# Performance work log

Measured on AMD Instinct MI355X. Metric: run time of the kernel, lower is better.

The kernel has to match this reference:

```python
import jax, jax.numpy as jnp
import numpy as np

N, F, H, E, G, C = 100000, 128, 128, 640000, 512, 6
EPS = 1e-5


def setup_inputs() -> dict:
    key = jax.random.key(0)
    ks = jax.random.split(key, 20)
    def w(k, shape, fan_in):
        return jax.random.normal(k, shape, jnp.float32) * (1.0 / np.sqrt(fan_in))
    return {
        "x": jax.random.normal(ks[0], (N, F), jnp.float32),
        "edge_index": jax.random.randint(ks[1], (2, E), 0, N),
        "batch": jnp.sort(jax.random.randint(ks[2], (N,), 0, G)),
        "num_graphs": G,
        # SAGEConv1: lin_l (aggregated, with bias) + lin_r (root, no bias)
        "W1l": w(ks[3], (F, H), F), "b1l": jnp.zeros((H,), jnp.float32), "W1r": w(ks[4], (F, H), F),
        # SAGEConv2
        "W2l": w(ks[5], (H, H), H), "b2l": jnp.zeros((H,), jnp.float32), "W2r": w(ks[6], (H, H), H),
        # cluster heads
        "Wc1": w(ks[7], (H, H), H), "bc1": jnp.zeros((H,), jnp.float32),
        "Wc2": w(ks[8], (H, 2), H), "bc2": jnp.zeros((2,), jnp.float32),
        # classifier
        "Wl1": w(ks[9], (H, H), H), "bl1": jnp.zeros((H,), jnp.float32),
        "Wl2": w(ks[10], (H, C), H), "bl2": jnp.zeros((C,), jnp.float32),
    }


def _sage(x, src, dst, Wl, bl, Wr):
    # PyG SAGEConv: mean-aggregate messages x[src] at dst, then lin_l(agg) + lin_r(x)
    n = x.shape[0]
    s = jax.ops.segment_sum(x[src], dst, num_segments=n)
    cnt = jax.ops.segment_sum(jnp.ones((src.shape[0],), x.dtype), dst, num_segments=n)
    agg = s / jnp.maximum(cnt, 1.0)[:, None]
    return agg @ Wl + bl + x @ Wr


def reference(x, edge_index, batch, num_graphs,
              W1l, b1l, W1r, W2l, b2l, W2r,
              Wc1, bc1, Wc2, bc2, Wl1, bl1, Wl2, bl2):
    src, dst = edge_index[0], edge_index[1]
    h = jax.nn.relu(_sage(x, src, dst, W1l, b1l, W1r))
    h = jax.nn.relu(_sage(h, src, dst, W2l, b2l, W2r))
    # 2-way soft cluster assignment per node
    a = jax.nn.softmax(jnp.tanh(h @ Wc1 + bc1) @ Wc2 + bc2, axis=1)  # [N,2]
    g = num_graphs
    # group_features[g] = a_g^T h_g  -> per-node outer product, segment-summed by graph
    gf = jax.ops.segment_sum(a[:, :, None] * h[:, None, :], batch, num_segments=g)  # [G,2,H]
    pos = gf[:, 0, :]  # positive-cluster embedding per graph
    # new_adj[g] = a_g^T A_g a_g ; only within-graph edges appear in the per-graph adj block
    same = (batch[src] == batch[dst]).astype(h.dtype)
    contrib = same[:, None, None] * (a[src][:, :, None] * a[dst][:, None, :])  # [E,2,2]
    new_adj = jax.ops.segment_sum(contrib, batch[src], num_segments=g)  # [G,2,2]
    # F.normalize(p=1, dim=1, eps=1e-5): row-wise L1 with clamped denominator
    l1 = jnp.sum(jnp.abs(new_adj), axis=2, keepdims=True)
    norm_adj = new_adj / jnp.maximum(l1, EPS)
    diag = jnp.diagonal(norm_adj, axis1=1, axis2=2)  # [G,2]
    penalty = jnp.mean(jnp.mean((diag - 1.0) ** 2, axis=1))  # mse vs ones(2), averaged over graphs
    # NOTE: original (faithfully reproduced) takes the mean over ALL nodes, same for every graph
    graph_emb = jnp.broadcast_to(jnp.mean(h, axis=0, keepdims=True), (g, h.shape[1]))
    z = jax.nn.relu(pos @ Wl1 + bl1)  # dropout off (eval mode)
    logits = z @ Wl2 + bl2
    return (jax.nn.log_softmax(logits, axis=-1), pos, graph_emb, penalty)
```

## Files before the change

kernel.cpp:

```cpp
#include <hip/hip_runtime.h>

#define NN 100000
#define NE 640000
#define HD 128
#define NG 512
#define NC 6
#define EPSV 1e-5f
#define OCT 12500

typedef __bf16 bf16_t;
typedef bf16_t bf16x8 __attribute__((ext_vector_type(8)));
typedef float f32x4 __attribute__((ext_vector_type(4)));

__device__ __forceinline__ float b2f(unsigned int u16) {
    return __builtin_bit_cast(float, u16 << 16);
}
__device__ __forceinline__ unsigned short f2b(float f) {
    unsigned int u = __builtin_bit_cast(unsigned int, f);
    unsigned int r = (u + 0x7fffu + ((u >> 16) & 1u)) >> 16;
    return (unsigned short)r;
}

__device__ __forceinline__ int frag_src(int i) {
    int g2 = i >> 6, ln = i & 63;
    int row = (g2 >> 2) * 16 + (ln & 15);
    return row * 16 + (g2 & 3) * 4 + (ln >> 4);
}

__global__ __launch_bounds__(256) void k_zero(uint4* __restrict__ p, int n16) {
    int i = blockIdx.x * 256 + threadIdx.x;
    if (i < n16) p[i] = (uint4){0u, 0u, 0u, 0u};
}

__global__ __launch_bounds__(256) void k_prep(
    const float* __restrict__ x, unsigned short* __restrict__ xb,
    const float* __restrict__ Wa, const float* __restrict__ Wb,
    const float* __restrict__ Wc, const float* __restrict__ Wd,
    const float* __restrict__ We, unsigned short* __restrict__ Wt,
    const int* __restrict__ dst, int* __restrict__ cnt)
{
    int bid = blockIdx.x;
    if (bid < 960) {
        int oct = bid & 7;
        int widx = bid >> 3;
        int lo = oct * OCT, hi = lo + OCT;
        for (int e = widx * 256 + threadIdx.x; e < NE; e += 120 * 256) {
            int d = dst[e];
            if (d >= lo && d < hi) atomicAdd(&cnt[d], 1);
        }
    } else if (bid < 7210) {
        int i = (bid - 960) * 256 + threadIdx.x;
        float4 v0 = reinterpret_cast<const float4*>(x)[i * 2];
        float4 v1 = reinterpret_cast<const float4*>(x)[i * 2 + 1];
        unsigned short u[8] = {f2b(v0.x), f2b(v0.y), f2b(v0.z), f2b(v0.w),
                               f2b(v1.x), f2b(v1.y), f2b(v1.z), f2b(v1.w)};
        reinterpret_cast<uint4*>(xb)[i] = *reinterpret_cast<uint4*>(u);
    } else {
        int i = (bid - 7210) * 256 + threadIdx.x;
        int w = i >> 14, r = i & 16383;
        int k = r >> 7, n = r & 127;
        const float* W = (w == 0) ? Wa : (w == 1) ? Wb : (w == 2) ? Wc : (w == 3) ? Wd : We;
        Wt[w * 16384 + n * HD + k] = f2b(W[k * HD + n]);
    }
}

__global__ void k_scan1(const int* __restrict__ cnt, int* __restrict__ excl,
                        int* __restrict__ bsum, int n) {
    __shared__ int sh[256];
    int i = blockIdx.x * 256 + threadIdx.x;
    int v = (i < n) ? cnt[i] : 0;
    sh[threadIdx.x] = v;
    __syncthreads();
    for (int off = 1; off < 256; off <<= 1) {
        int t = (threadIdx.x >= off) ? sh[threadIdx.x - off] : 0;
        __syncthreads();
        sh[threadIdx.x] += t;
        __syncthreads();
    }
    if (i < n) excl[i] = sh[threadIdx.x] - v;
    if (threadIdx.x == 255) bsum[blockIdx.x] = sh[255];
}

__global__ void k_scan2(int* bsum, int nb) {
    __shared__ int sh[512];
    int t = threadIdx.x;
    sh[t] = (t < nb) ? bsum[t] : 0;
    __syncthreads();
    for (int off = 1; off < 512; off <<= 1) {
        int v = (t >= off) ? sh[t - off] : 0;
        __syncthreads();
        sh[t] += v;
        __syncthreads();
    }
    if (t < nb) bsum[t] = sh[t];
}

__global__ void k_scan3(const int* __restrict__ excl, const int* __restrict__ bsum,
                        int* __restrict__ row_off, int n) {
    int i = blockIdx.x * 256 + threadIdx.x;
    if (i < n) row_off[i] = excl[i] + (blockIdx.x ? bsum[blockIdx.x - 1] : 0);
    if (i == 0) row_off[n] = NE;
}

__global__ __launch_bounds__(256) void k_fill(const int* __restrict__ src,
                                              const int* __restrict__ dst,
                                              const int* __restrict__ row_off,
                                              int* __restrict__ cnt,
                                              int* __restrict__ csr) {
    int q = blockIdx.x;
    int oct = q & 7;
    int widx = q >> 3;
    int lo = oct * OCT, hi = lo + OCT;
    for (int e = widx * 256 + threadIdx.x; e < NE; e += 120 * 256) {
        int d = dst[e];
        if (d >= lo && d < hi) {
            int p = atomicSub(&cnt[d], 1);
            csr[row_off[d] + p - 1] = src[e];
        }
    }
}

__global__ __launch_bounds__(512) void k_sage(
    const unsigned short* __restrict__ X,
    const int* __restrict__ row_off, const int* __restrict__ csr,
    const unsigned short* __restrict__ Wlt, const unsigned short* __restrict__ Wrt,
    const float* __restrict__ bias, unsigned short* __restrict__ out, int M)
{
    __shared__ uint4 wlds[4096];
    const int wid = threadIdx.x >> 6;
    const int lane = threadIdx.x & 63;
    const int lrow = lane & 15;
    const int lkg = lane >> 4;
    const int r0 = blockIdx.x * 128 + wid * 16;

    const uint4* gl = reinterpret_cast<const uint4*>(Wlt);
    const uint4* gr = reinterpret_cast<const uint4*>(Wrt);
    for (int i = threadIdx.x; i < 2048; i += 512) {
        int si = frag_src(i);
        wlds[i] = gl[si];
        wlds[2048 + i] = gr[si];
    }

    int row = r0 + lrow;
    row = row < M ? row : M - 1;
    int beg = row_off[row], end = row_off[row + 1];

    float accg[4][8];
#pragma unroll
    for (int ks = 0; ks < 4; ++ks)
#pragma unroll
        for (int j = 0; j < 8; ++j) accg[ks][j] = 0.f;

    const unsigned short* Xk = X + lkg * 8;
    for (int j = beg; j < end; j += 2) {
        int s0 = csr[j];
        const unsigned short* p0 = Xk + (size_t)s0 * HD;
        uint4 w0 = *reinterpret_cast<const uint4*>(p0);
        uint4 w1 = *reinterpret_cast<const uint4*>(p0 + 32);
        uint4 w2 = *reinterpret_cast<const uint4*>(p0 + 64);
        uint4 w3 = *reinterpret_cast<const uint4*>(p0 + 96);
        bool ok1 = (j + 1) < end;
        int s1 = csr[ok1 ? j + 1 : j];
        const unsigned short* p1 = Xk + (size_t)s1 * HD;
        uint4 y0, y1, y2, y3;
        if (ok1) {
            y0 = *reinterpret_cast<const uint4*>(p1);
            y1 = *reinterpret_cast<const uint4*>(p1 + 32);
            y2 = *reinterpret_cast<const uint4*>(p1 + 64);
            y3 = *reinterpret_cast<const uint4*>(p1 + 96);
        }
        accg[0][0] += b2f(w0.x & 0xffffu); accg[0][1] += b2f(w0.x >> 16);
        accg[0][2] += b2f(w0.y & 0xffffu); accg[0][3] += b2f(w0.y >> 16);
        accg[0][4] += b2f(w0.z & 0xffffu); accg[0][5] += b2f(w0.z >> 16);
        accg[0][6] += b2f(w0.w & 0xffffu); accg[0][7] += b2f(w0.w >> 16);
        accg[1][0] += b2f(w1.x & 0xffffu); accg[1][1] += b2f(w1.x >> 16);
        accg[1][2] += b2f(w1.y & 0xffffu); accg[1][3] += b2f(w1.y >> 16);
        accg[1][4] += b2f(w1.z & 0xffffu); accg[1][5] += b2f(w1.z >> 16);
        accg[1][6] += b2f(w1.w & 0xffffu); accg[1][7] += b2f(w1.w >> 16);
        accg[2][0] += b2f(w2.x & 0xffffu); accg[2][1] += b2f(w2.x >> 16);
        accg[2][2] += b2f(w2.y & 0xffffu); accg[2][3] += b2f(w2.y >> 16);
        accg[2][4] += b2f(w2.z & 0xffffu); accg[2][5] += b2f(w2.z >> 16);
        accg[2][6] += b2f(w2.w & 0xffffu); accg[2][7] += b2f(w2.w >> 16);
        accg[3][0] += b2f(w3.x & 0xffffu); accg[3][1] += b2f(w3.x >> 16);
        accg[3][2] += b2f(w3.y & 0xffffu); accg[3][3] += b2f(w3.y >> 16);
        accg[3][4] += b2f(w3.z & 0xffffu); accg[3][5] += b2f(w3.z >> 16);
        accg[3][6] += b2f(w3.w & 0xffffu); accg[3][7] += b2f(w3.w >> 16);
        if (ok1) {
            accg[0][0] += b2f(y0.x & 0xffffu); accg[0][1] += b2f(y0.x >> 16);
            accg[0][2] += b2f(y0.y & 0xffffu); accg[0][3] += b2f(y0.y >> 16);
            accg[0][4] += b2f(y0.z & 0xffffu); accg[0][5] += b2f(y0.z >> 16);
            accg[0][6] += b2f(y0.w & 0xffffu); accg[0][7] += b2f(y0.w >> 16);
            accg[1][0] += b2f(y1.x & 0xffffu); accg[1][1] += b2f(y1.x >> 16);
            accg[1][2] += b2f(y1.y & 0xffffu); accg[1][3] += b2f(y1.y >> 16);
            accg[1][4] += b2f(y1.z & 0xffffu); accg[1][5] += b2f(y1.z >> 16);
            accg[1][6] += b2f(y1.w & 0xffffu); accg[1][7] += b2f(y1.w >> 16);
            accg[2][0] += b2f(y2.x & 0xffffu); accg[2][1] += b2f(y2.x >> 16);
            accg[2][2] += b2f(y2.y & 0xffffu); accg[2][3] += b2f(y2.y >> 16);
            accg[2][4] += b2f(y2.z & 0xffffu); accg[2][5] += b2f(y2.z >> 16);
            accg[2][6] += b2f(y2.w & 0xffffu); accg[2][7] += b2f(y2.w >> 16);
            accg[3][0] += b2f(y3.x & 0xffffu); accg[3][1] += b2f(y3.x >> 16);
            accg[3][2] += b2f(y3.y & 0xffffu); accg[3][3] += b2f(y3.y >> 16);
            accg[3][4] += b2f(y3.z & 0xffffu); accg[3][5] += b2f(y3.z >> 16);
            accg[3][6] += b2f(y3.w & 0xffffu); accg[3][7] += b2f(y3.w >> 16);
        }
    }

    float inv = 1.f / fmaxf((float)(end - beg), 1.f);
    bf16x8 a1[4], a2f[4];
#pragma unroll
    for (int ks = 0; ks < 4; ++ks) {
        unsigned short u[8];
#pragma unroll
        for (int j = 0; j < 8; ++j) u[j] = f2b(accg[ks][j] * inv);
        a1[ks] = *reinterpret_cast<bf16x8*>(u);
    }
    const unsigned short* p2 = X + (size_t)row * HD + lkg * 8;
#pragma unroll
    for (int ks = 0; ks < 4; ++ks)
        a2f[ks] = *reinterpret_cast<const bf16x8*>(p2 + ks * 32);

    f32x4 acc[8];
#pragma unroll
    for (int t = 0; t < 8; ++t) {
        float b = bias[t * 16 + lrow];
        acc[t] = (f32x4){b, b, b, b};
    }

    __syncthreads();

#pragma unroll
    for (int ks = 0; ks < 4; ++ks) {
#pragma unroll
        for (int t = 0; t < 8; ++t) {
            int fi = (t * 4 + ks) * 64 + lane;
            bf16x8 bl = __builtin_bit_cast(bf16x8, wlds[fi]);
            bf16x8 br = __builtin_bit_cast(bf16x8, wlds[2048 + fi]);
            acc[t] = __builtin_amdgcn_mfma_f32_16x16x32_bf16(a1[ks], bl, acc[t], 0, 0, 0);
            acc[t] = __builtin_amdgcn_mfma_f32_16x16x32_bf16(a2f[ks], br, acc[t], 0, 0, 0);
        }
    }

#pragma unroll
    for (int t = 0; t < 8; ++t)
#pragma unroll
        for (int r = 0; r < 4; ++r) {
            int orow = r0 + lkg * 4 + r;
            if (orow < M)
                out[(size_t)orow * HD + t * 16 + lrow] = f2b(fmaxf(acc[t][r], 0.f));
        }
}

__global__ __launch_bounds__(256) void mfma_attn(
    const unsigned short* __restrict__ A1, const unsigned short* __restrict__ W1t,
    const float* __restrict__ bias, const float* __restrict__ Wc2,
    const float* __restrict__ bc2, float* __restrict__ a2, int M)
{
    __shared__ uint4 wlds[2048];
    const int wid = threadIdx.x >> 6;
    const int lane = threadIdx.x & 63;
    const int lrow = lane & 15;
    const int lkg = lane >> 4;
    const int r0 = blockIdx.x * 128 + wid * 32;

    const uint4* g4 = reinterpret_cast<const uint4*>(W1t);
    for (int i = threadIdx.x; i < 2048; i += 256)
        wlds[i] = g4[frag_src(i)];

    bf16x8 a[2][4];
#pragma unroll
    for (int g = 0; g < 2; ++g) {
        int row = r0 + g * 16 + lrow;
        row = row < M ? row : M - 1;
        const unsigned short* p = A1 + (size_t)row * HD + lkg * 8;
#pragma unroll
        for (int ks = 0; ks < 4; ++ks)
            a[g][ks] = *reinterpret_cast<const bf16x8*>(p + ks * 32);
    }

    f32x4 acc[2][8];
#pragma unroll
    for (int t = 0; t < 8; ++t) {
        float b = bias[t * 16 + lrow];
        acc[0][t] = (f32x4){b, b, b, b};
        acc[1][t] = (f32x4){b, b, b, b};
    }

    __syncthreads();

#pragma unroll
    for (int ks = 0; ks < 4; ++ks) {
#pragma unroll
        for (int t = 0; t < 8; ++t) {
            bf16x8 b = __builtin_bit_cast(bf16x8, wlds[(t * 4 + ks) * 64 + lane]);
            acc[0][t] = __builtin_amdgcn_mfma_f32_16x16x32_bf16(a[0][ks], b, acc[0][t], 0, 0, 0);
            acc[1][t] = __builtin_amdgcn_mfma_f32_16x16x32_bf16(a[1][ks], b, acc[1][t], 0, 0, 0);
        }
    }

    float p0[2][4] = {{0.f, 0.f, 0.f, 0.f}, {0.f, 0.f, 0.f, 0.f}};
    float p1[2][4] = {{0.f, 0.f, 0.f, 0.f}, {0.f, 0.f, 0.f, 0.f}};
#pragma unroll
    for (int t = 0; t < 8; ++t) {
        float2 wv = reinterpret_cast<const float2*>(Wc2)[t * 16 + lrow];
#pragma unroll
        for (int g = 0; g < 2; ++g)
#pragma unroll
            for (int r = 0; r < 4; ++r) {
                float tv = tanhf(acc[g][t][r]);
                p0[g][r] = fmaf(tv, wv.x, p0[g][r]);
                p1[g][r] = fmaf(tv, wv.y, p1[g][r]);
            }
    }
#pragma unroll
    for (int off = 1; off < 16; off <<= 1) {
#pragma unroll
        for (int g = 0; g < 2; ++g)
#pragma unroll
            for (int r = 0; r < 4; ++r) {
                p0[g][r] += __shfl_xor(p0[g][r], off, 64);
                p1[g][r] += __shfl_xor(p1[g][r], off, 64);
            }
    }
    if (lrow == 0) {
        float B0 = bc2[0], B1 = bc2[1];
#pragma unroll
        for (int g = 0; g < 2; ++g)
#pragma unroll
            for (int r = 0; r < 4; ++r) {
                int row = r0 + g * 16 + lkg * 4 + r;
                if (row < M) {
                    float u0 = p0[g][r] + B0, u1 = p1[g][r] + B1;
                    float m = fmaxf(u0, u1);
                    float e0 = expf(u0 - m), e1 = expf(u1 - m);
                    float inv = 1.f / (e0 + e1);
                    reinterpret_cast<float2*>(a2)[row] = (float2){e0 * inv, e1 * inv};
                }
            }
    }
}

__global__ __launch_bounds__(1024) void k_posadj(const unsigned short* __restrict__ h,
                                                 const float* __restrict__ a2,
                                                 const int* __restrict__ batch,
                                                 const int* __restrict__ src,
                                                 const int* __restrict__ dst,
                                                 float* __restrict__ pos_out,
                                                 float* __restrict__ csum,
                                                 float* __restrict__ adj) {
    __shared__ float4 sh[16][64];
    __shared__ float shadj[NG * 4];
    int bid = blockIdx.x;
    if (bid < NG) {
        int g = bid;
        int lo = 0, hi = NN;
        while (lo < hi) { int m = (lo + hi) >> 1; if (batch[m] < g) lo = m + 1; else hi = m; }
        int beg = lo;
        hi = NN;
        while (lo < hi) { int m = (lo + hi) >> 1; if (batch[m] < g + 1) lo = m + 1; else hi = m; }
        int end = lo;
        int grp = threadIdx.x >> 6;
        int lane = threadIdx.x & 63;
        float4 acc = {0.f, 0.f, 0.f, 0.f};
        for (int i = beg + grp * 2; i < end; i += 32) {
            int i1 = i + 1;
            bool ok1 = i1 < end;
            float a0 = a2[i * 2];
            unsigned int v0 = *reinterpret_cast<const unsigned int*>(h + (size_t)i * HD + lane * 2);
            float a1 = ok1 ? a2[i1 * 2] : 0.f;
            unsigned int v1 = ok1 ? *reinterpret_cast<const unsigned int*>(h + (size_t)i1 * HD + lane * 2) : 0u;
            float f0 = b2f(v0 & 0xffffu), f1 = b2f(v0 >> 16);
            float g0 = b2f(v1 & 0xffffu), g1 = b2f(v1 >> 16);
            acc.x = fmaf(a0, f0, fmaf(a1, g0, acc.x));
            acc.y = fmaf(a0, f1, fmaf(a1, g1, acc.y));
            acc.z += f0 + g0;
            acc.w += f1 + g1;
        }
        sh[grp][lane] = acc;
        __syncthreads();
        if (threadIdx.x < 64) {
            float4 s = sh[0][lane];
#pragma unroll
            for (int k = 1; k < 16; ++k) {
                float4 t = sh[k][lane];
                s.x += t.x; s.y += t.y; s.z += t.z; s.w += t.w;
            }
            reinterpret_cast<float2*>(pos_out)[g * 64 + lane] = (float2){s.x, s.y};
            atomicAdd(&csum[lane * 2], s.z);
            atomicAdd(&csum[lane * 2 + 1], s.w);
        }
    } else {
        for (int i = threadIdx.x; i < NG * 4; i += 1024) shadj[i] = 0.f;
        __syncthreads();
        for (int e = (bid - NG) * 1024 + threadIdx.x; e < NE; e += 120 * 1024) {
            int s = src[e], d = dst[e];
            int bs = batch[s], bd = batch[d];
            if (bs != bd) continue;
            float a0s = a2[2 * s], a1s = a2[2 * s + 1];
            float a0d = a2[2 * d], a1d = a2[2 * d + 1];
            float* A = shadj + bs * 4;
            atomicAdd(A + 0, a0s * a0d);
            atomicAdd(A + 1, a0s * a1d);
            atomicAdd(A + 2, a1s * a0d);
            atomicAdd(A + 3, a1s * a1d);
        }
        __syncthreads();
        for (int i = threadIdx.x; i < NG * 4; i += 1024) {
            float v = shadj[i];
            if (v != 0.f) atomicAdd(&adj[i], v);
        }
    }
}

__global__ __launch_bounds__(512) void k_tail(const float* __restrict__ csum,
                                              float* __restrict__ gemb_out,
                                              const float* __restrict__ adj,
                                              float* __restrict__ pen) {
    int bid = blockIdx.x;
    if (bid < 128) {
        int i = bid * 512 + threadIdx.x;
        gemb_out[i] = csum[i & 127] * (1.f / (float)NN);
    } else {
        __shared__ float sh[512];
        int g = threadIdx.x;
        float x0 = adj[g * 4], x1 = adj[g * 4 + 1], x2 = adj[g * 4 + 2], x3 = adj[g * 4 + 3];
        float l0 = fabsf(x0) + fabsf(x1);
        float l1 = fabsf(x2) + fabsf(x3);
        float d0 = x0 / fmaxf(l0, EPSV);
        float d1 = x3 / fmaxf(l1, EPSV);
        sh[g] = 0.5f * ((d0 - 1.f) * (d0 - 1.f) + (d1 - 1.f) * (d1 - 1.f));
        __syncthreads();
        for (int off = 256; off >= 1; off >>= 1) {
            if (g < off) sh[g] += sh[g + off];
            __syncthreads();
        }
        if (g == 0) pen[0] = sh[0] * (1.f / (float)NG);
    }
}

__global__ __launch_bounds__(256) void gemm_head(
    const float* __restrict__ A, const float* __restrict__ W,
    const float* __restrict__ bias, float* __restrict__ out, int M)
{
    const int tid = threadIdx.x;
    const int w = __builtin_amdgcn_readfirstlane(tid >> 6);
    const int lane = tid & 63;
    const int r0 = blockIdx.x * 32 + w * 8;
    if (r0 >= M) return;
    const int c0 = lane, c1 = lane + 64;
    float acc0[8], acc1[8];
    const float b0 = bias[c0], b1 = bias[c1];
#pragma unroll
    for (int r = 0; r < 8; ++r) { acc0[r] = b0; acc1[r] = b1; }
    const float* Ap = A + (size_t)r0 * HD;
    for (int k4 = 0; k4 < HD / 4; ++k4) {
        float4 a[8];
#pragma unroll
        for (int r = 0; r < 8; ++r)
            a[r] = *reinterpret_cast<const float4*>(Ap + r * HD + k4 * 4);
#pragma unroll
        for (int j = 0; j < 4; ++j) {
            const int k = k4 * 4 + j;
            const float w0 = W[k * HD + c0];
            const float w1 = W[k * HD + c1];
#pragma unroll
            for (int r = 0; r < 8; ++r) {
                const float av = (j == 0) ? a[r].x : (j == 1) ? a[r].y
                               : (j == 2) ? a[r].z : a[r].w;
                acc0[r] = fmaf(av, w0, acc0[r]);
                acc1[r] = fmaf(av, w1, acc1[r]);
            }
        }
    }
#pragma unroll
    for (int r = 0; r < 8; ++r) {
        out[(size_t)(r0 + r) * HD + c0] = fmaxf(acc0[r], 0.f);
        out[(size_t)(r0 + r) * HD + c1] = fmaxf(acc1[r], 0.f);
    }
}

__global__ void k_head(const float* __restrict__ z, const float* __restrict__ Wl2,
                       const float* __restrict__ bl2, float* __restrict__ out0) {
    int g = blockIdx.x * blockDim.x + threadIdx.x;
    if (g >= NG) return;
    float l[NC];
#pragma unroll
    for (int c = 0; c < NC; ++c) l[c] = bl2[c];
    for (int k = 0; k < HD; ++k) {
        float zv = z[(size_t)g * HD + k];
#pragma unroll
        for (int c = 0; c < NC; ++c) l[c] = fmaf(zv, Wl2[k * NC + c], l[c]);
    }
    float m = l[0];
#pragma unroll
    for (int c = 1; c < NC; ++c) m = fmaxf(m, l[c]);
    float sum = 0.f;
#pragma unroll
    for (int c = 0; c < NC; ++c) sum += expf(l[c] - m);
    float lse = m + logf(sum);
#pragma unroll
    for (int c = 0; c < NC; ++c) out0[g * NC + c] = l[c] - lse;
}

extern "C" void kernel_launch(void* const* d_in, const int* in_sizes, int n_in,
                              void* d_out, int out_size, void* d_ws, size_t ws_size,
                              hipStream_t stream) {
    const float* x   = (const float*)d_in[0];
    const int*   ei  = (const int*)d_in[1];
    const int*   src = ei;
    const int*   dst = ei + NE;
    const int*   batch = (const int*)d_in[2];
    const float* W1l = (const float*)d_in[4];
    const float* b1l = (const float*)d_in[5];
    const float* W1r = (const float*)d_in[6];
    const float* W2l = (const float*)d_in[7];
    const float* b2l = (const float*)d_in[8];
    const float* W2r = (const float*)d_in[9];
    const float* Wc1 = (const float*)d_in[10];
    const float* bc1 = (const float*)d_in[11];
    const float* Wc2 = (const float*)d_in[12];
    const float* bc2 = (const float*)d_in[13];
    const float* Wl1 = (const float*)d_in[14];
    const float* bl1 = (const float*)d_in[15];
    const float* Wl2 = (const float*)d_in[16];
    const float* bl2 = (const float*)d_in[17];

    char* ws = (char*)d_ws;
    const size_t BB = (size_t)NN * HD * 2;
    unsigned short* xb   = (unsigned short*)(ws);
    unsigned short* bufB = (unsigned short*)(ws + BB);
    size_t O = 2 * BB;
    int*   cnt     = (int*)(ws + O);
    float* adj     = (float*)(ws + O + 400000);
    float* csum    = (float*)(ws + O + 408192);
    int*   row_off = (int*)(ws + O + 408704);
    int*   excl    = (int*)(ws + O + 808768);
    int*   bsum    = (int*)(ws + O + 1208768);
    int*   csr     = (int*)(ws + O + 1212864);
    float* a2      = (float*)(ws + O + 3772864);
    float* zbuf    = (float*)(ws + O + 4572864);
    unsigned short* w1lt = (unsigned short*)(ws + O + 4835008);
    unsigned short* w1rt = w1lt + 16384;
    unsigned short* w2lt = w1rt + 16384;
    unsigned short* w2rt = w2lt + 16384;
    unsigned short* wc1t = w2rt + 16384;

    float* out0 = (float*)d_out;
    float* pos  = out0 + NG * NC;
    float* gemb = pos + NG * HD;
    float* pen  = gemb + NG * HD;

    k_zero<<<100, 256, 0, stream>>>((uint4*)(ws + O), 25544);
    k_prep<<<7530, 256, 0, stream>>>(x, xb, W1l, W1r, W2l, W2r, Wc1, w1lt, dst, cnt);
    k_scan1<<<391, 256, 0, stream>>>(cnt, excl, bsum, NN);
    k_scan2<<<1, 512, 0, stream>>>(bsum, 391);
    k_scan3<<<391, 256, 0, stream>>>(excl, bsum, row_off, NN);
    k_fill<<<960, 256, 0, stream>>>(src, dst, row_off, cnt, csr);

    const int SAGE_GRID = (NN + 127) / 128;
    k_sage<<<SAGE_GRID, 512, 0, stream>>>(xb, row_off, csr, w1lt, w1rt, b1l, bufB, NN);
    k_sage<<<SAGE_GRID, 512, 0, stream>>>(bufB, row_off, csr, w2lt, w2rt, b2l, xb, NN);
    mfma_attn<<<(NN + 127) / 128, 256, 0, stream>>>(xb, wc1t, bc1, Wc2, bc2, a2, NN);
    k_posadj<<<NG + 120, 1024, 0, stream>>>(xb, a2, batch, src, dst, pos, csum, adj);
    k_tail<<<129, 512, 0, stream>>>(csum, gemb, adj, pen);
    gemm_head<<<NG / 32, 256, 0, stream>>>(pos, Wl1, bl1, zbuf, NG);
    k_head<<<2, 256, 0, stream>>>(zbuf, Wl2, bl2, out0);
}
```

Before: 276.9 us.

## Split SAGE kernel weight staging into two column halves to halve LDS

```diff
diff --git a/kernel.cpp b/kernel.cpp
--- a/kernel.cpp
+++ b/kernel.cpp
@@ -19,6 +19,12 @@
     unsigned int u = __builtin_bit_cast(unsigned int, f);
     unsigned int r = (u + 0x7fffu + ((u >> 16) & 1u)) >> 16;
     return (unsigned short)r;
+}
+
+__device__ __forceinline__ int frag_src_h(int i, int h) {
+    int g2 = i >> 6, ln = i & 63;
+    int row = (h * 4 + (g2 >> 2)) * 16 + (ln & 15);
+    return row * 16 + (g2 & 3) * 4 + (ln >> 4);
 }
 
 __device__ __forceinline__ int frag_src(int i) {
@@ -126,7 +132,7 @@
     const unsigned short* __restrict__ Wlt, const unsigned short* __restrict__ Wrt,
     const float* __restrict__ bias, unsigned short* __restrict__ out, int M)
 {
-    __shared__ uint4 wlds[4096];
+    __shared__ uint4 wlds[2048];
     const int wid = threadIdx.x >> 6;
     const int lane = threadIdx.x & 63;
     const int lrow = lane & 15;
@@ -135,10 +141,9 @@
 
     const uint4* gl = reinterpret_cast<const uint4*>(Wlt);
     const uint4* gr = reinterpret_cast<const uint4*>(Wrt);
-    for (int i = threadIdx.x; i < 2048; i += 512) {
-        int si = frag_src(i);
-        wlds[i] = gl[si];
-        wlds[2048 + i] = gr[si];
+    for (int i = threadIdx.x; i < 1024; i += 512) {
+        wlds[i] = gl[frag_src_h(i, 0)];
+        wlds[1024 + i] = gr[frag_src_h(i, 0)];
     }
 
     int row = r0 + lrow;
@@ -219,35 +224,68 @@
     for (int ks = 0; ks < 4; ++ks)
         a2f[ks] = *reinterpret_cast<const bf16x8*>(p2 + ks * 32);
 
-    f32x4 acc[8];
-#pragma unroll
-    for (int t = 0; t < 8; ++t) {
-        float b = bias[t * 16 + lrow];
-        acc[t] = (f32x4){b, b, b, b};
+    {
+        f32x4 acc[4];
+#pragma unroll
+        for (int t = 0; t < 4; ++t) {
+            float b = bias[t * 16 + lrow];
+            acc[t] = (f32x4){b, b, b, b};
+        }
+        __syncthreads();
+#pragma unroll
+        for (int ks = 0; ks < 4; ++ks) {
+#pragma unroll
+            for (int t = 0; t < 4; ++t) {
+                int fi = (t * 4 + ks) * 64 + lane;
+                bf16x8 bl = __builtin_bit_cast(bf16x8, wlds[fi]);
+                bf16x8 br = __builtin_bit_cast(bf16x8, wlds[1024 + fi]);
+                acc[t] = __builtin_amdgcn_mfma_f32_16x16x32_bf16(a1[ks], bl, acc[t], 0, 0, 0);
+                acc[t] = __builtin_amdgcn_mfma_f32_16x16x32_bf16(a2f[ks], br, acc[t], 0, 0, 0);
+            }
+        }
+#pragma unroll
+        for (int t = 0; t < 4; ++t)
+#pragma unroll
+            for (int r = 0; r < 4; ++r) {
+                int orow = r0 + lkg * 4 + r;
+                if (orow < M)
+                    out[(size_t)orow * HD + t * 16 + lrow] = f2b(fmaxf(acc[t][r], 0.f));
+            }
     }
 
     __syncthreads();
-
-#pragma unroll
-    for (int ks = 0; ks < 4; ++ks) {
-#pragma unroll
-        for (int t = 0; t < 8; ++t) {
-            int fi = (t * 4 + ks) * 64 + lane;
-            bf16x8 bl = __builtin_bit_cast(bf16x8, wlds[fi]);
-            bf16x8 br = __builtin_bit_cast(bf16x8, wlds[2048 + fi]);
-            acc[t] = __builtin_amdgcn_mfma_f32_16x16x32_bf16(a1[ks], bl, acc[t], 0, 0, 0);
-            acc[t] = __builtin_amdgcn_mfma_f32_16x16x32_bf16(a2f[ks], br, acc[t], 0, 0, 0);
-        }
-    }
-
-#pragma unroll
-    for (int t = 0; t < 8; ++t)
-#pragma unroll
-        for (int r = 0; r < 4; ++r) {
-            int orow = r0 + lkg * 4 + r;
-            if (orow < M)
-                out[(size_t)orow * HD + t * 16 + lrow] = f2b(fmaxf(acc[t][r], 0.f));
-        }
+    for (int i = threadIdx.x; i < 1024; i += 512) {
+        wlds[i] = gl[frag_src_h(i, 1)];
+        wlds[1024 + i] = gr[frag_src_h(i, 1)];
+    }
+    {
+        f32x4 acc[4];
+#pragma unroll
+        for (int t = 0; t < 4; ++t) {
+            float b = bias[(4 + t) * 16 + lrow];
+            acc[t] = (f32x4){b, b, b, b};
+        }
+        __syncthreads();
+#pragma unroll
+        for (int ks = 0; ks < 4; ++ks) {
+#pragma unroll
+            for (int t = 0; t < 4; ++t) {
+                int fi = (t * 4 + ks) * 64 + lane;
+                bf16x8 bl = __builtin_bit_cast(bf16x8, wlds[fi]);
+                bf16x8 br = __builtin_bit_cast(bf16x8, wlds[1024 + fi]);
+                acc[t] = __builtin_amdgcn_mfma_f32_16x16x32_bf16(a1[ks], bl, acc[t], 0, 0, 0);
+                acc[t] = __builtin_amdgcn_mfma_f32_16x16x32_bf16(a2f[ks], br, acc[t], 0, 0, 0);
+            }
+        }
+#pragma unroll
+        for (int t = 0; t < 4; ++t)
+#pragma unroll
+            for (int r = 0; r < 4; ++r) {
+                int orow = r0 + lkg * 4 + r;
+                if (orow < M)
+                    out[(size_t)orow * HD + (4 + t) * 16 + lrow] = f2b(fmaxf(acc[t][r], 0.f));
+            }
+    }
 }
 
 __global__ __launch_bounds__(256) void mfma_attn(
```

After: 276.2 us. Within noise of the previous version (-0.2%).
